# Optimization experiments

Measured on AMD Instinct MI355X. Metric: run time of the kernel, lower is better.

## Reference

```python
import jax, jax.numpy as jnp
import numpy as np


def setup_inputs() -> dict:
    key = jax.random.key(0)
    kq, kk, kv, km = jax.random.split(key, 4)
    B, H, S, D = 2, 16, 2048, 64
    queries = jax.random.normal(kq, (B, H, S, D), dtype=jnp.float32)
    keys = jax.random.normal(kk, (B, H, S, D), dtype=jnp.float32)
    values = jax.random.normal(kv, (B, H, S, D), dtype=jnp.float32)
    # additive binary mask (1 = masked position), broadcast over batch/heads
    mask = jax.random.randint(km, (1, 1, S, S), 0, 2, dtype=jnp.int32)
    return {"queries": queries, "keys": keys, "values": values,
            "mask": mask, "key_dim": D}


def reference(queries, keys, values, mask, key_dim):
    # scores = Q K^T / sqrt(d)   -> [B, H, S, S]
    scale = 1.0 / jnp.sqrt(jnp.asarray(key_dim, dtype=jnp.float32))
    scores = jnp.einsum('bhqd,bhkd->bhqk', queries, keys) * scale
    # additive mask: masked positions get -1e9
    scores = scores + (-1.0e9) * mask.astype(scores.dtype)
    weights = jax.nn.softmax(scores, axis=-1)
    # attention output: weights @ V -> [B, H, S, D]
    return jnp.einsum('bhqk,bhkd->bhqd', weights, values)
```

## Files before the change

### kernel.cpp

```cpp
#include <hip/hip_runtime.h>

typedef __attribute__((ext_vector_type(8))) short short8;
typedef __attribute__((ext_vector_type(4))) float floatx4;
typedef __attribute__((ext_vector_type(4))) unsigned short ushort4v;

#define S_LEN 2048
#define D_HEAD 64
#define NT64 (S_LEN / 64)
#define PITCH 72
#define TP 73
#define SCALE2 0.18033688f
#define MASK_BIAS2 -2.0e9f

static __device__ __forceinline__ unsigned short f2bf(float f) {
  unsigned int x = __builtin_bit_cast(unsigned int, f);
  x += 0x7fffu + ((x >> 16) & 1u);
  return (unsigned short)(x >> 16);
}
static __device__ __forceinline__ float bf2f(unsigned short u) {
  unsigned int x = ((unsigned int)u) << 16;
  return __builtin_bit_cast(float, x);
}
static __device__ __forceinline__ short8 cvt8(const float* __restrict__ p) {
  float4 a = *(const float4*)p;
  float4 b = *(const float4*)(p + 4);
  short8 r;
  r[0] = (short)f2bf(a.x); r[1] = (short)f2bf(a.y);
  r[2] = (short)f2bf(a.z); r[3] = (short)f2bf(a.w);
  r[4] = (short)f2bf(b.x); r[5] = (short)f2bf(b.y);
  r[6] = (short)f2bf(b.z); r[7] = (short)f2bf(b.w);
  return r;
}
static __device__ __forceinline__ short8 cvt8s(const float* __restrict__ p) {
  float4 a = *(const float4*)p;
  float4 b = *(const float4*)(p + 4);
  short8 r;
  r[0] = (short)f2bf(a.x * SCALE2); r[1] = (short)f2bf(a.y * SCALE2);
  r[2] = (short)f2bf(a.z * SCALE2); r[3] = (short)f2bf(a.w * SCALE2);
  r[4] = (short)f2bf(b.x * SCALE2); r[5] = (short)f2bf(b.y * SCALE2);
  r[6] = (short)f2bf(b.z * SCALE2); r[7] = (short)f2bf(b.w * SCALE2);
  return r;
}
static __device__ __forceinline__ void cp16(const void* g, void* l) {
  __builtin_amdgcn_global_load_lds(
      (const __attribute__((address_space(1))) unsigned int*)g,
      (__attribute__((address_space(3))) unsigned int*)l, 16, 0, 0);
}
static __device__ __forceinline__ unsigned int pk2f(float a, float b) {
  const unsigned int ab = __builtin_bit_cast(unsigned int, a) + 0x8000u;
  const unsigned int bb = __builtin_bit_cast(unsigned int, b) + 0x8000u;
  return __builtin_amdgcn_perm(bb, ab, 0x07060302u);
}

__global__ __launch_bounds__(256) void prep(
    const float* __restrict__ K, const float* __restrict__ V,
    const int* __restrict__ mask,
    unsigned short* __restrict__ Kws, unsigned short* __restrict__ Vws,
    unsigned long long* __restrict__ Mb, int BH)
{
  __shared__ unsigned short t[D_HEAD * TP];
  const int tid = threadIdx.x;
  const int nbK = BH * 64;
  const int nbV = BH * 32;
  int b = blockIdx.x;

  if (b < nbK) {
    const int tt   = b * 256 + tid;
    const int bh   = tt >> 14;
    const int rem  = tt & 16383;
    const int tile = rem >> 9;
    const int n    = rem & 511;
    const int row  = n >> 3;
    const int col8 = (n & 7) ^ (row & 7);
    short8 r = cvt8(K + ((size_t)(bh * S_LEN + tile * 64 + row)) * D_HEAD + col8 * 8);
    *(short8*)(Kws + (size_t)tt * 8) = r;
    return;
  }
  b -= nbK;
  if (b < nbV) {
    const int tile = b & 31;
    const int bh   = b >> 5;
    const int s0   = tile * 64;
    const float* Vb = V + (size_t)bh * S_LEN * D_HEAD;
#pragma unroll
    for (int p = 0; p < 4; ++p) {
      const int s  = p * 16 + (tid >> 4);
      const int d0 = (tid & 15) * 4;
      float4 v = *(const float4*)(Vb + (size_t)(s0 + s) * D_HEAD + d0);
      unsigned short* dst = &t[s * TP + d0];
      dst[0] = f2bf(v.x); dst[1] = f2bf(v.y); dst[2] = f2bf(v.z); dst[3] = f2bf(v.w);
    }
    __syncthreads();
    unsigned short* Vo = Vws + ((size_t)(bh * 32 + tile)) * 4096;
#pragma unroll
    for (int p = 0; p < 2; ++p) {
      const int n    = p * 256 + tid;
      const int d    = n >> 3;
      const int col8 = (n & 7) ^ (d & 7);
      short8 r;
#pragma unroll
      for (int j = 0; j < 8; ++j) r[j] = (short)t[(col8 * 8 + j) * TP + d];
      *(short8*)(Vo + (size_t)n * 8) = r;
    }
    return;
  }
  b -= nbV;
  const int rg   = b >> 2;
  const int cq   = b & 3;
  const int lane = tid & 63;
  const int row  = rg * 4 + (tid >> 6);
#pragma unroll 8
  for (int c = cq * 8; c < cq * 8 + 8; ++c) {
    const int mv = mask[(size_t)row * S_LEN + c * 64 + lane];
    const unsigned long long bm = __ballot(mv != 0);
    if (lane == 0) Mb[(size_t)row * NT64 + c] = bm;
  }
}

__global__ __launch_bounds__(256, 3) void fa_fwd9(
    const float* __restrict__ Q,
    const unsigned short* __restrict__ Kws,
    const unsigned short* __restrict__ Vws,
    const unsigned long long* __restrict__ Mb,
    float* __restrict__ Out)
{
  __shared__ unsigned short Kbuf[2][64 * 64];
  __shared__ unsigned short Vbuf[2][64 * 64];
  __shared__ unsigned short Plds[4][32 * 64];

  const int tid  = threadIdx.x;
  const int wv   = tid >> 6;
  const int lane = tid & 63;
  const int quad = lane >> 4;
  const int l16  = lane & 15;
  const int l8   = l16 & 7;

  const int bh = blockIdx.y;
  const int qw = blockIdx.x * 128 + wv * 32;

  const float* Qb = Q + (size_t)bh * S_LEN * D_HEAD;
  const unsigned short* KT = Kws + (size_t)bh * NT64 * 4096;
  const unsigned short* VT = Vws + (size_t)bh * NT64 * 4096;

  short8 qfrag[2][2];
#pragma unroll
  for (int g = 0; g < 2; ++g)
#pragma unroll
    for (int w = 0; w < 2; ++w)
      qfrag[g][w] = cvt8s(Qb + (size_t)(qw + g * 16 + l16) * D_HEAD + w * 32 + quad * 8);

  short8 kones;
#pragma unroll
  for (int j = 0; j < 8; ++j) kones[j] = (short)0x3F80;

  floatx4 ot[2][4];
#pragma unroll
  for (int g = 0; g < 2; ++g)
#pragma unroll
    for (int dt = 0; dt < 4; ++dt) ot[g][dt] = (floatx4){0.f, 0.f, 0.f, 0.f};
  floatx4 lacc[2];
  lacc[0] = (floatx4){0.f, 0.f, 0.f, 0.f};
  lacc[1] = (floatx4){0.f, 0.f, 0.f, 0.f};

  unsigned short* pl = &Plds[wv][0];
  const unsigned long long* mrowp[2];
#pragma unroll
  for (int g = 0; g < 2; ++g)
    mrowp[g] = Mb + (size_t)(qw + g * 16 + l16) * NT64;

  auto stage = [&](int kt, int buf) {
#pragma unroll
    for (int j = 0; j < 2; ++j) {
      const int c0 = (wv * 2 + j) * 64;
      cp16(KT + (size_t)kt * 4096 + (size_t)(c0 + lane) * 8, &Kbuf[buf][c0 * 8]);
      cp16(VT + (size_t)kt * 4096 + (size_t)(c0 + lane) * 8, &Vbuf[buf][c0 * 8]);
    }
  };

  stage(0, 0);
  __syncthreads();

  for (int kt = 0; kt < NT64; ++kt) {
    const int cur = kt & 1;
    if (kt + 1 < NT64) stage(kt + 1, cur ^ 1);
    const unsigned short* Kl = Kbuf[cur];
    const unsigned short* Vl = Vbuf[cur];

    floatx4 st[2][4];
#pragma unroll
    for (int g = 0; g < 2; ++g)
#pragma unroll
      for (int nt = 0; nt < 4; ++nt) st[g][nt] = (floatx4){0.f, 0.f, 0.f, 0.f};
#pragma unroll
    for (int w = 0; w < 2; ++w)
#pragma unroll
      for (int nt = 0; nt < 4; ++nt) {
        short8 kf = *(const short8*)&Kl[(nt * 16 + l16) * 64 + (((w * 4 + quad) ^ l8) * 8)];
        st[0][nt] = __builtin_amdgcn_mfma_f32_16x16x32_bf16(kf, qfrag[0][w], st[0][nt], 0, 0, 0);
        st[1][nt] = __builtin_amdgcn_mfma_f32_16x16x32_bf16(kf, qfrag[1][w], st[1][nt], 0, 0, 0);
      }

#pragma unroll
    for (int g = 0; g < 2; ++g) {
      const unsigned long long mw = mrowp[g][kt];
#pragma unroll
      for (int nt = 0; nt < 4; ++nt) {
        const unsigned nib = (unsigned)(mw >> (nt * 16 + quad * 4)) & 0xFu;
        float p[4];
#pragma unroll
        for (int r = 0; r < 4; ++r) {
          float pv = __builtin_amdgcn_exp2f(st[g][nt][r]);
          p[r] = ((nib >> r) & 1u) ? 0.0f : pv;
        }
        const unsigned int d0 = pk2f(p[0], p[1]);
        const unsigned int d1 = pk2f(p[2], p[3]);
        const int c = nt * 2 + (quad >> 1);
        unsigned int* dst = (unsigned int*)&pl[(g * 16 + l16) * 64 + ((c ^ l8) * 8) + (quad & 1) * 4];
        dst[0] = d0; dst[1] = d1;
      }
    }

#pragma unroll
    for (int w = 0; w < 2; ++w) {
      short8 pf0 = *(const short8*)&pl[(l16) * 64 + (((w * 4 + quad) ^ l8) * 8)];
      short8 pf1 = *(const short8*)&pl[(16 + l16) * 64 + (((w * 4 + quad) ^ l8) * 8)];
      lacc[0] = __builtin_amdgcn_mfma_f32_16x16x32_bf16(kones, pf0, lacc[0], 0, 0, 0);
      lacc[1] = __builtin_amdgcn_mfma_f32_16x16x32_bf16(kones, pf1, lacc[1], 0, 0, 0);
#pragma unroll
      for (int dt = 0; dt < 4; ++dt) {
        short8 vf = *(const short8*)&Vl[(dt * 16 + l16) * 64 + (((w * 4 + quad) ^ l8) * 8)];
        ot[0][dt] = __builtin_amdgcn_mfma_f32_16x16x32_bf16(vf, pf0, ot[0][dt], 0, 0, 0);
        ot[1][dt] = __builtin_amdgcn_mfma_f32_16x16x32_bf16(vf, pf1, ot[1][dt], 0, 0, 0);
      }
    }
    __syncthreads();
  }

#pragma unroll
  for (int g = 0; g < 2; ++g) {
    const float invl = 1.0f / lacc[g][0];
    float* Ob = Out + (size_t)bh * S_LEN * D_HEAD + (size_t)(qw + g * 16 + l16) * D_HEAD;
#pragma unroll
    for (int dt = 0; dt < 4; ++dt) {
      float4 v;
      v.x = ot[g][dt][0] * invl; v.y = ot[g][dt][1] * invl;
      v.z = ot[g][dt][2] * invl; v.w = ot[g][dt][3] * invl;
      *(float4*)(Ob + dt * 16 + quad * 4) = v;
    }
  }
}

__global__ __launch_bounds__(256) void fa_fwd(
    const float* __restrict__ Q, const float* __restrict__ K, const float* __restrict__ V,
    const int* __restrict__ mask, float* __restrict__ Out)
{
  __shared__ unsigned short Vt[D_HEAD * PITCH];
  __shared__ unsigned short Plds[4][16 * PITCH];
  const int tid = threadIdx.x, wv = tid >> 6, lane = tid & 63, quad = lane >> 4, l16 = lane & 15;
  const int bh = blockIdx.y, qw = blockIdx.x * 64 + wv * 16;
  const float* Qb = Q + (size_t)bh * S_LEN * D_HEAD;
  const float* Kb = K + (size_t)bh * S_LEN * D_HEAD;
  const float* Vb = V + (size_t)bh * S_LEN * D_HEAD;
  short8 qfrag[2];
#pragma unroll
  for (int w = 0; w < 2; ++w)
    qfrag[w] = cvt8(Qb + (size_t)(qw + l16) * D_HEAD + w * 32 + quad * 8);
  floatx4 o[4];
#pragma unroll
  for (int nt = 0; nt < 4; ++nt) o[nt] = (floatx4){0.f, 0.f, 0.f, 0.f};
  float m_run[4], l_run[4];
#pragma unroll
  for (int r = 0; r < 4; ++r) { m_run[r] = -1.0e30f; l_run[r] = 0.f; }
  unsigned short* pl = &Plds[wv][0];
  for (int kt = 0; kt < NT64; ++kt) {
    const int k0 = kt * 64;
    __syncthreads();
#pragma unroll
    for (int it = 0; it < 2; ++it) {
      const int s = it * 32 + (tid >> 3), d0 = (tid & 7) * 8, dblk = (tid & 7);
      const int swz = (((s >> 3) ^ dblk) & 7) * 8 + (s & 7);
      const float* vp = Vb + (size_t)(k0 + s) * D_HEAD + d0;
      float4 a = *(const float4*)vp; float4 bb = *(const float4*)(vp + 4);
      const float vvv[8] = {a.x, a.y, a.z, a.w, bb.x, bb.y, bb.z, bb.w};
#pragma unroll
      for (int j = 0; j < 8; ++j) Vt[(d0 + j) * PITCH + swz] = f2bf(vvv[j]);
    }
    __syncthreads();
    floatx4 scf[4];
#pragma unroll
    for (int nt = 0; nt < 4; ++nt) scf[nt] = (floatx4){0.f, 0.f, 0.f, 0.f};
#pragma unroll
    for (int w = 0; w < 2; ++w)
#pragma unroll
      for (int nt = 0; nt < 4; ++nt) {
        short8 kf = cvt8(Kb + (size_t)(k0 + nt * 16 + l16) * D_HEAD + w * 32 + quad * 8);
        scf[nt] = __builtin_amdgcn_mfma_f32_16x16x32_bf16(qfrag[w], kf, scf[nt], 0, 0, 0);
      }
    float s_val[4][4], mloc[4] = {-1.0e30f, -1.0e30f, -1.0e30f, -1.0e30f};
#pragma unroll
    for (int nt = 0; nt < 4; ++nt)
#pragma unroll
      for (int r = 0; r < 4; ++r) {
        const int mk = mask[(size_t)(qw + quad * 4 + r) * S_LEN + (k0 + nt * 16 + l16)];
        const float sv = scf[nt][r] * SCALE2 + (mk ? MASK_BIAS2 : 0.0f);
        s_val[nt][r] = sv; mloc[r] = fmaxf(mloc[r], sv);
      }
#pragma unroll
    for (int r = 0; r < 4; ++r)
#pragma unroll
      for (int off = 1; off < 16; off <<= 1) mloc[r] = fmaxf(mloc[r], __shfl_xor(mloc[r], off));
    float alpha[4], rsum[4];
#pragma unroll
    for (int r = 0; r < 4; ++r) {
      const float mnew = fmaxf(m_run[r], mloc[r]);
      alpha[r] = exp2f(m_run[r] - mnew); m_run[r] = mnew; rsum[r] = 0.f;
    }
#pragma unroll
    for (int nt = 0; nt < 4; ++nt)
#pragma unroll
      for (int r = 0; r < 4; ++r) {
        const float p = exp2f(s_val[nt][r] - m_run[r]);
        const unsigned short ph = f2bf(p);
        rsum[r] += bf2f(ph);
        pl[(quad * 4 + r) * PITCH + nt * 16 + l16] = ph;
      }
    __syncthreads();
#pragma unroll
    for (int r = 0; r < 4; ++r) {
#pragma unroll
      for (int off = 1; off < 16; off <<= 1) rsum[r] += __shfl_xor(rsum[r], off);
      l_run[r] = l_run[r] * alpha[r] + rsum[r];
    }
#pragma unroll
    for (int nt = 0; nt < 4; ++nt)
#pragma unroll
      for (int r = 0; r < 4; ++r) o[nt][r] *= alpha[r];
#pragma unroll
    for (int w = 0; w < 2; ++w) {
      short8 af = *(const short8*)&pl[l16 * PITCH + w * 32 + quad * 8];
#pragma unroll
      for (int nt = 0; nt < 4; ++nt) {
        const int d = nt * 16 + l16, blk = ((w * 4 + quad) ^ (d >> 3)) & 7;
        short8 vf = *(const short8*)&Vt[d * PITCH + blk * 8];
        o[nt] = __builtin_amdgcn_mfma_f32_16x16x32_bf16(af, vf, o[nt], 0, 0, 0);
      }
    }
  }
  float invl[4];
#pragma unroll
  for (int r = 0; r < 4; ++r) invl[r] = 1.0f / l_run[r];
  float* Ob = Out + (size_t)bh * S_LEN * D_HEAD;
#pragma unroll
  for (int nt = 0; nt < 4; ++nt)
#pragma unroll
    for (int r = 0; r < 4; ++r)
      Ob[(size_t)(qw + quad * 4 + r) * D_HEAD + nt * 16 + l16] = o[nt][r] * invl[r];
}

extern "C" void kernel_launch(void* const* d_in, const int* in_sizes, int n_in,
                              void* d_out, int out_size, void* d_ws, size_t ws_size,
                              hipStream_t stream) {
  const float* Q = (const float*)d_in[0];
  const float* K = (const float*)d_in[1];
  const float* V = (const float*)d_in[2];
  const int* mask = (const int*)d_in[3];
  float* Out = (float*)d_out;
  const int BH = in_sizes[0] / (S_LEN * D_HEAD);
  const size_t NH = (size_t)BH * S_LEN * D_HEAD;
  const size_t nMb = (size_t)S_LEN * NT64;
  const size_t need = NH * 2 * 2 + nMb * 8;

  if (ws_size >= need) {
    unsigned short* Kws = (unsigned short*)d_ws;
    unsigned short* Vws = Kws + NH;
    unsigned long long* Mbits = (unsigned long long*)(Vws + NH);
    const int nbPrep = BH * 64 + BH * 32 + S_LEN;
    prep<<<dim3(nbPrep), 256, 0, stream>>>(K, V, mask, Kws, Vws, Mbits, BH);
    fa_fwd9<<<dim3(S_LEN / 128, BH), 256, 0, stream>>>(Q, Kws, Vws, Mbits, Out);
  } else {
    fa_fwd<<<dim3(S_LEN / 64, BH), 256, 0, stream>>>(Q, K, V, mask, Out);
  }
}
```

Before: 167.3 us.

## Triple-buffer K/V staging with vmcnt waits, setprio, and XCD-aware block swizzle

Moves the K/V LDS staging from double to triple buffering, prefetching two tiles ahead and replacing __syncthreads with explicit vmcnt waits plus s_barrier so loads for later tiles stay in flight. MFMA phases are wrapped in s_setprio to favour matrix issue across waves. The grid is flattened and swizzled so consecutive blocks on each XCD share the same head for L2 reuse of K/V. The extra LDS buffers cut occupancy from 3 to 2 blocks per CU, and the hand-counted vmcnt values must match the number of outstanding cp16 loads.

```diff
diff --git a/kernel.cpp b/kernel.cpp
--- a/kernel.cpp
+++ b/kernel.cpp
@@ -117,15 +117,15 @@
   }
 }
 
-__global__ __launch_bounds__(256, 3) void fa_fwd9(
+__global__ __launch_bounds__(256, 2) void fa_fwd9(
     const float* __restrict__ Q,
     const unsigned short* __restrict__ Kws,
     const unsigned short* __restrict__ Vws,
     const unsigned long long* __restrict__ Mb,
     float* __restrict__ Out)
 {
-  __shared__ unsigned short Kbuf[2][64 * 64];
-  __shared__ unsigned short Vbuf[2][64 * 64];
+  __shared__ unsigned short Kbuf[3][64 * 64];
+  __shared__ unsigned short Vbuf[3][64 * 64];
   __shared__ unsigned short Plds[4][32 * 64];
 
   const int tid  = threadIdx.x;
@@ -135,12 +135,27 @@
   const int l16  = lane & 15;
   const int l8   = l16 & 7;
 
-  const int bh = blockIdx.y;
-  const int qw = blockIdx.x * 128 + wv * 32;
+  const int nwg  = gridDim.x;
+  const int flat = blockIdx.x;
+  const int swz  = (flat & 7) * (nwg >> 3) + (flat >> 3);
+  const int bh   = swz >> 4;
+  const int qw   = (swz & 15) * 128 + wv * 32;
 
   const float* Qb = Q + (size_t)bh * S_LEN * D_HEAD;
   const unsigned short* KT = Kws + (size_t)bh * NT64 * 4096;
   const unsigned short* VT = Vws + (size_t)bh * NT64 * 4096;
+
+  auto stage = [&](int kt, int buf) {
+#pragma unroll
+    for (int j = 0; j < 2; ++j) {
+      const int c0 = (wv * 2 + j) * 64;
+      cp16(KT + (size_t)kt * 4096 + (size_t)(c0 + lane) * 8, &Kbuf[buf][c0 * 8]);
+      cp16(VT + (size_t)kt * 4096 + (size_t)(c0 + lane) * 8, &Vbuf[buf][c0 * 8]);
+    }
+  };
+
+  stage(0, 0);
+  stage(1, 1);
 
   short8 qfrag[2][2];
 #pragma unroll
@@ -168,21 +183,13 @@
   for (int g = 0; g < 2; ++g)
     mrowp[g] = Mb + (size_t)(qw + g * 16 + l16) * NT64;
 
-  auto stage = [&](int kt, int buf) {
-#pragma unroll
-    for (int j = 0; j < 2; ++j) {
-      const int c0 = (wv * 2 + j) * 64;
-      cp16(KT + (size_t)kt * 4096 + (size_t)(c0 + lane) * 8, &Kbuf[buf][c0 * 8]);
-      cp16(VT + (size_t)kt * 4096 + (size_t)(c0 + lane) * 8, &Vbuf[buf][c0 * 8]);
-    }
-  };
-
-  stage(0, 0);
-  __syncthreads();
-
+  asm volatile("s_waitcnt vmcnt(4)" ::: "memory");
+  __builtin_amdgcn_s_barrier();
+
+  int cur = 0;
   for (int kt = 0; kt < NT64; ++kt) {
-    const int cur = kt & 1;
-    if (kt + 1 < NT64) stage(kt + 1, cur ^ 1);
+    const int sb = cur == 0 ? 2 : cur - 1;
+    if (kt + 2 < NT64) stage(kt + 2, sb);
     const unsigned short* Kl = Kbuf[cur];
     const unsigned short* Vl = Vbuf[cur];
 
@@ -191,6 +198,7 @@
     for (int g = 0; g < 2; ++g)
 #pragma unroll
       for (int nt = 0; nt < 4; ++nt) st[g][nt] = (floatx4){0.f, 0.f, 0.f, 0.f};
+    __builtin_amdgcn_s_setprio(1);
 #pragma unroll
     for (int w = 0; w < 2; ++w)
 #pragma unroll
@@ -199,6 +207,7 @@
         st[0][nt] = __builtin_amdgcn_mfma_f32_16x16x32_bf16(kf, qfrag[0][w], st[0][nt], 0, 0, 0);
         st[1][nt] = __builtin_amdgcn_mfma_f32_16x16x32_bf16(kf, qfrag[1][w], st[1][nt], 0, 0, 0);
       }
+    __builtin_amdgcn_s_setprio(0);
 
 #pragma unroll
     for (int g = 0; g < 2; ++g) {
@@ -220,6 +229,7 @@
       }
     }
 
+    __builtin_amdgcn_s_setprio(1);
 #pragma unroll
     for (int w = 0; w < 2; ++w) {
       short8 pf0 = *(const short8*)&pl[(l16) * 64 + (((w * 4 + quad) ^ l8) * 8)];
@@ -233,7 +243,16 @@
         ot[1][dt] = __builtin_amdgcn_mfma_f32_16x16x32_bf16(vf, pf1, ot[1][dt], 0, 0, 0);
       }
     }
-    __syncthreads();
+    __builtin_amdgcn_s_setprio(0);
+
+    if (kt + 2 < NT64) {
+      asm volatile("s_waitcnt vmcnt(4)" ::: "memory");
+      __builtin_amdgcn_s_barrier();
+    } else if (kt + 1 < NT64) {
+      asm volatile("s_waitcnt vmcnt(0)" ::: "memory");
+      __builtin_amdgcn_s_barrier();
+    }
+    cur = cur == 2 ? 0 : cur + 1;
   }
 
 #pragma unroll
@@ -376,7 +395,7 @@
     unsigned long long* Mbits = (unsigned long long*)(Vws + NH);
     const int nbPrep = BH * 64 + BH * 32 + S_LEN;
     prep<<<dim3(nbPrep), 256, 0, stream>>>(K, V, mask, Kws, Vws, Mbits, BH);
-    fa_fwd9<<<dim3(S_LEN / 128, BH), 256, 0, stream>>>(Q, Kws, Vws, Mbits, Out);
+    fa_fwd9<<<dim3((S_LEN / 128) * BH), 256, 0, stream>>>(Q, Kws, Vws, Mbits, Out);
   } else {
     fa_fwd<<<dim3(S_LEN / 64, BH), 256, 0, stream>>>(Q, K, V, mask, Out);
   }
```

Result: no change. 168.5 us (+0.8%).
